# Kernel tuning notes

Hardware: AMD Instinct MI355X
Metric: run time of the kernel (lower is better)

The kernel has to match this reference:

```python
import jax, jax.numpy as jnp
import numpy as np

NB = 4
QN = -(2 ** (NB - 1))   # -8
QP = 2 ** (NB - 1) - 1  # 7
EPS = 1e-5


def _grad_scale(x, g):
    # forward: x, backward: grad * g (LSQ gradient scaling)
    return x * g + jax.lax.stop_gradient(x - x * g)


def _round_pass(x):
    # round with straight-through estimator
    return x + jax.lax.stop_gradient(jnp.round(x) - x)


def _lsq(v, alpha, qn, qp):
    # LSQ fake quantize-dequantize with learnable step size alpha
    g = 1.0 / np.sqrt(v.size * qp)
    a = _grad_scale(alpha, g)
    return _round_pass(jnp.clip(v / a, qn, qp)) * a


def _bn(x, g, b, m, v):
    # eval-mode BatchNorm2d over channel dim of NCHW
    s = (g * jax.lax.rsqrt(v + EPS))[None, :, None, None]
    return (x - m[None, :, None, None]) * s + b[None, :, None, None]


def _conv(x, w, stride, pad, groups):
    return jax.lax.conv_general_dilated(
        x, w, (stride, stride), pad,
        dimension_numbers=('NCHW', 'OIHW', 'NCHW'),
        feature_group_count=groups)


def setup_inputs() -> dict:
    key = jax.random.key(0)
    ks = jax.random.split(key, 4)
    inp, oup, hid = 96, 96, 576
    B, H, W = 32, 28, 28
    d = {}
    d['x'] = jax.random.normal(ks[0], (B, inp, H, W), jnp.float32)
    d['w1'] = jax.random.normal(ks[1], (hid, inp, 1, 1), jnp.float32) * 0.1
    d['w2'] = jax.random.normal(ks[2], (hid, 1, 3, 3), jnp.float32) * 0.1
    d['w3'] = jax.random.normal(ks[3], (oup, hid, 1, 1), jnp.float32) * 0.1
    for i, c in zip((1, 2, 3), (hid, hid, oup)):
        d[f'aw{i}'] = jnp.full((1,), 0.05, jnp.float32)  # weight step size
        d[f'ax{i}'] = jnp.full((1,), 0.5, jnp.float32)   # activation step size
        d[f'g{i}'] = jnp.ones((c,), jnp.float32)
        d[f'b{i}'] = jnp.zeros((c,), jnp.float32)
        d[f'm{i}'] = jnp.zeros((c,), jnp.float32)
        d[f'v{i}'] = jnp.ones((c,), jnp.float32)
    return d


def reference(x, w1, w2, w3, aw1, ax1, g1, b1, m1, v1,
              aw2, ax2, g2, b2, m2, v2, aw3, ax3, g3, b3, m3, v3):
    hid = w1.shape[0]
    # 1x1 expand conv (LSQ on activation and weight)
    h = _conv(_lsq(x, ax1, QN, QP), _lsq(w1, aw1, QN, QP), 1, [(0, 0), (0, 0)], 1)
    h = jnp.clip(_bn(h, g1, b1, m1, v1), 0.0, 6.0)
    # 3x3 depthwise conv, stride 1
    h = _conv(_lsq(h, ax2, QN, QP), _lsq(w2, aw2, QN, QP), 1, [(1, 1), (1, 1)], hid)
    h = jnp.clip(_bn(h, g2, b2, m2, v2), 0.0, 6.0)
    # 1x1 project conv
    h = _conv(_lsq(h, ax3, QN, QP), _lsq(w3, aw3, QN, QP), 1, [(0, 0), (0, 0)], 1)
    h = _bn(h, g3, b3, m3, v3)
    # identity residual (stride==1 and inp==oup)
    return x + h
```

## Files before the change

kernel.cpp:

```cpp
#include <hip/hip_runtime.h>

#define EPSF 1e-5f

typedef int    int4v   __attribute__((ext_vector_type(4)));
typedef float  float4v __attribute__((ext_vector_type(4)));

#define W1P_OFF  0
#define W3P_OFF  55296
#define W2D_OFF  110592
#define S1B1_OFF 202752
#define S2B2_OFF 207360
#define S3B3_OFF 211968

#define H1S 296
#define H2S 600

__device__ __forceinline__ float lsq_q(float v, float a) {
    float t = v / a;
    t = fminf(fmaxf(t, -8.0f), 7.0f);
    return rintf(t);
}

__device__ __forceinline__ long q8pack_w(const float* w, int base, const int* idx, float a) {
    unsigned long long v = 0;
    #pragma unroll
    for (int j = 0; j < 8; ++j) {
        int q = (int)lsq_q(w[base + idx[j]], a);
        v |= (unsigned long long)(q & 255) << (8 * j);
    }
    return (long)v;
}

__global__ __launch_bounds__(256)
void prep_w(const float* __restrict__ w1, const float* __restrict__ w2,
            const float* __restrict__ w3,
            const float* aw1, const float* ax1, const float* ax2,
            const float* aw2, const float* ax3, const float* aw3,
            const float* __restrict__ g1, const float* __restrict__ b1,
            const float* __restrict__ m1, const float* __restrict__ v1,
            const float* __restrict__ g2, const float* __restrict__ b2,
            const float* __restrict__ m2, const float* __restrict__ v2,
            const float* __restrict__ g3, const float* __restrict__ b3,
            const float* __restrict__ m3, const float* __restrict__ v3,
            long* __restrict__ w1p, long* __restrict__ w3p,
            long* __restrict__ w2d,
            float* __restrict__ s1b1, float* __restrict__ s2b2,
            float* __restrict__ s3b3) {
    int id = blockIdx.x * 256 + threadIdx.x;
    const int lin[8] = {0, 1, 2, 3, 4, 5, 6, 7};
    if (id < 6912) {
        int l = id & 63, t = id >> 6;
        int kc = t % 3, ct = t / 3;
        int co = ct * 16 + (l & 15);
        int ci0 = kc * 32 + (l >> 4) * 8;
        w1p[id] = q8pack_w(w1, co * 96 + ci0, lin, aw1[0]);
    } else if (id < 13824) {
        int i = id - 6912;
        int l = i & 63, t = i >> 6;
        int kc = t % 18, ct = t / 18;
        int co = ct * 16 + (l & 15);
        int ci0 = kc * 32 + (l >> 4) * 8;
        w3p[i] = q8pack_w(w3, co * 576 + ci0, lin, aw3[0]);
    } else if (id < 25344) {
        int i = id - 13824;
        int l = i & 63, t = i >> 6;
        int kc = t % 5, ct = t / 5;
        int quad = l >> 4, m = l & 15;
        int tap = kc * 2 + (quad >> 1);
        unsigned long long v = 0;
        if (tap <= 8) {
            int mh = m - (quad & 1) * 8;
            if (mh >= 0 && mh < 8) {
                int j = (mh >> 1) | ((mh & 1) << 2);
                int q = (int)lsq_q(w2[(ct * 16 + m) * 9 + tap], aw2[0]);
                v = (unsigned long long)(unsigned)(q & 255) << (8 * j);
            }
        }
        w2d[i] = (long)v;
    } else if (id < 25920) {
        int c = id - 25344;
        float s = g1[c] / sqrtf(v1[c] + EPSF);
        float A = aw1[0] * ax1[0];
        float inv = 1.0f / ax2[0];
        s1b1[c] = A * s * inv;
        s1b1[576 + c] = (b1[c] - m1[c] * s) * inv;
    } else if (id < 26496) {
        int c = id - 25920;
        float s = g2[c] / sqrtf(v2[c] + EPSF);
        float A = ax2[0] * aw2[0];
        float inv = 1.0f / ax3[0];
        s2b2[c] = A * s * inv;
        s2b2[576 + c] = (b2[c] - m2[c] * s) * inv;
    } else if (id < 26592) {
        int c = id - 26496;
        float s = g3[c] / sqrtf(v3[c] + EPSF);
        float A = ax3[0] * aw3[0];
        s3b3[c] = A * s;
        s3b3[96 + c] = b3[c] - m3[c] * s;
    }
}

__global__ __launch_bounds__(448, 4)
void fused_k(const float* __restrict__ x, const long* __restrict__ w1p,
             const long* __restrict__ w2d, const long* __restrict__ w3p,
             const float* __restrict__ ax1,
             const float* __restrict__ s1b1, const float* __restrict__ s2b2,
             const float* __restrict__ s3b3, float* __restrict__ out) {
    __shared__ __align__(16) signed char h1[120 * H1S];
    __shared__ __align__(16) signed char h2[64 * H2S];
    const int tid = threadIdx.x;
    const int w = tid >> 6, l = tid & 63;
    const int quad = l >> 4, c16 = l & 15;
    const int qh = quad >> 1, ql = quad & 1;
    const int b = blockIdx.x;
    const int r0 = blockIdx.y * 2;

    for (int i = tid; i < 120 * H1S / 16; i += 448)
        ((int4v*)h1)[i] = (int4v){0, 0, 0, 0};
    __syncthreads();

    {
        const int lp = w * 16 + c16;
        const int row = lp / 28, col = lp - (lp / 28) * 28;
        const int img_row = r0 - 1 + row;
        const bool valid = (unsigned)img_row < 28u;
        const int p = min(max(img_row, 0), 27) * 28 + col;
        const float inv1 = 1.0f / ax1[0];

        long bfr[3];
        #pragma unroll
        for (int kc = 0; kc < 3; ++kc) {
            const float* xs = x + (b * 96 + kc * 32 + quad * 8) * 784 + p;
            unsigned long long v = 0;
            #pragma unroll
            for (int j = 0; j < 8; ++j) {
                float t = xs[j * 784] * inv1;
                t = fminf(fmaxf(t, -8.0f), 7.0f);
                int q = (int)rintf(t);
                v |= (unsigned long long)(q & 255) << (8 * j);
            }
            bfr[kc] = (long)v;
        }
        const int pos_h = row * 30 + col + 1;
        #pragma unroll 4
        for (int ct = 0; ct < 36; ++ct) {
            int4v acc; acc[0] = 0; acc[1] = 0; acc[2] = 0; acc[3] = 0;
            #pragma unroll
            for (int kc = 0; kc < 3; ++kc)
                acc = __builtin_amdgcn_mfma_i32_16x16x32_i8(
                    w1p[(ct * 3 + kc) * 64 + l], bfr[kc], acc, 0, 0, 0);
            const int co0 = ct * 16 + quad * 4;
            float4v S = *(const float4v*)(s1b1 + co0);
            float4v B = *(const float4v*)(s1b1 + 576 + co0);
            int pk = 0;
            #pragma unroll
            for (int r = 0; r < 4; ++r) {
                float t = fmaf((float)acc[r], S[r], B[r]);
                t = fminf(fmaxf(t, 0.0f), 7.0f);
                pk |= ((int)rintf(t)) << (4 * r);
            }
            if (valid)
                *(unsigned short*)(h1 + pos_h * H1S + (co0 >> 1)) = (unsigned short)pk;
        }
    }
    __syncthreads();

    for (int t = w; t < 144; t += 7) {
        const int pt = t / 36, ct = t - (t / 36) * 36;
        const int pos = pt * 16 + c16;
        const int posc = min(pos, 55);
        const int row_in = posc / 28, col = posc - (posc / 28) * 28;
        const int choff = ct * 8 + ql * 4;
        int4v acc; acc[0] = 0; acc[1] = 0; acc[2] = 0; acc[3] = 0;
        #pragma unroll
        for (int kc = 0; kc < 5; ++kc) {
            int tap = kc * 2 + qh;
            tap = min(tap, 8);
            const int dh = tap / 3 - 1, dc = tap - (tap / 3) * 3 - 1;
            const int pos_h = (row_in + 1 + dh) * 30 + (col + 1 + dc);
            const unsigned v = *(const unsigned*)(h1 + pos_h * H1S + choff);
            const unsigned lo = v & 0x0F0F0F0Fu;
            const unsigned hi = (v >> 4) & 0x0F0F0F0Fu;
            const long bf = (long)(((unsigned long long)hi << 32) | lo);
            acc = __builtin_amdgcn_mfma_i32_16x16x32_i8(
                w2d[(ct * 5 + kc) * 64 + l], bf, acc, 0, 0, 0);
        }
        if (pos < 56) {
            const int c0 = ct * 16 + quad * 4;
            float4v S = *(const float4v*)(s2b2 + c0);
            float4v B = *(const float4v*)(s2b2 + 576 + c0);
            int pk = 0;
            #pragma unroll
            for (int r = 0; r < 4; ++r) {
                float tt = fmaf((float)acc[r], S[r], B[r]);
                tt = fminf(fmaxf(tt, 0.0f), 7.0f);
                pk |= ((int)rintf(tt)) << (8 * r);
            }
            *(int*)(h2 + pos * H2S + c0) = pk;
        }
    }
    __syncthreads();

    for (int t = w; t < 24; t += 7) {
        const int nt = t / 6, ct = t - (t / 6) * 6;
        int4v acc; acc[0] = 0; acc[1] = 0; acc[2] = 0; acc[3] = 0;
        const signed char* arow = h2 + (nt * 16 + c16) * H2S + quad * 8;
        #pragma unroll 6
        for (int kc = 0; kc < 18; ++kc)
            acc = __builtin_amdgcn_mfma_i32_16x16x32_i8(
                *(const long*)(arow + kc * 32),
                w3p[(ct * 18 + kc) * 64 + l], acc, 0, 0, 0);
        const int nloc = nt * 16 + quad * 4;
        if (nloc < 56) {
            const int co = ct * 16 + c16;
            const float S = s3b3[co], Bv = s3b3[96 + co];
            const int off = (b * 96 + co) * 784 + r0 * 28 + nloc;
            const float4v xr = *(const float4v*)(x + off);
            float4v o;
            #pragma unroll
            for (int r = 0; r < 4; ++r)
                o[r] = fmaf((float)acc[r], S, Bv) + xr[r];
            *(float4v*)(out + off) = o;
        }
    }
}

extern "C" void kernel_launch(void* const* d_in, const int* in_sizes, int n_in,
                              void* d_out, int out_size, void* d_ws, size_t ws_size,
                              hipStream_t stream) {
    const float* x   = (const float*)d_in[0];
    const float* w1  = (const float*)d_in[1];
    const float* w2  = (const float*)d_in[2];
    const float* w3  = (const float*)d_in[3];
    const float* aw1 = (const float*)d_in[4];
    const float* ax1 = (const float*)d_in[5];
    const float* g1  = (const float*)d_in[6];
    const float* b1  = (const float*)d_in[7];
    const float* m1  = (const float*)d_in[8];
    const float* v1  = (const float*)d_in[9];
    const float* aw2 = (const float*)d_in[10];
    const float* ax2 = (const float*)d_in[11];
    const float* g2  = (const float*)d_in[12];
    const float* b2  = (const float*)d_in[13];
    const float* m2  = (const float*)d_in[14];
    const float* v2  = (const float*)d_in[15];
    const float* aw3 = (const float*)d_in[16];
    const float* ax3 = (const float*)d_in[17];
    const float* g3  = (const float*)d_in[18];
    const float* b3  = (const float*)d_in[19];
    const float* m3  = (const float*)d_in[20];
    const float* v3  = (const float*)d_in[21];

    char* ws = (char*)d_ws;
    long* w1p = (long*)(ws + W1P_OFF);
    long* w3p = (long*)(ws + W3P_OFF);
    long* w2d = (long*)(ws + W2D_OFF);
    float* s1b1 = (float*)(ws + S1B1_OFF);
    float* s2b2 = (float*)(ws + S2B2_OFF);
    float* s3b3 = (float*)(ws + S3B3_OFF);

    float* out = (float*)d_out;

    prep_w<<<104, 256, 0, stream>>>(w1, w2, w3, aw1, ax1, ax2, aw2, ax3, aw3,
                                    g1, b1, m1, v1, g2, b2, m2, v2, g3, b3, m3, v3,
                                    w1p, w3p, w2d, s1b1, s2b2, s3b3);
    dim3 grid(32, 14);
    fused_k<<<grid, 448, 0, stream>>>(x, w1p, w2d, w3p, ax1, s1b1, s2b2, s3b3, out);
}
```

Measured before the change: 145.0 us.

## Split fused block into expand-conv kernel and depthwise+project kernel via global buffer

The expand 1x1 conv moves out of the fused kernel into its own kernel, which writes packed 4-bit activations to a global workspace in NHWC layout. The depthwise+project kernel then handles one output row per block and loads the needed halo rows from that buffer. This removes the redundant recomputation of halo rows in the expand conv (previously 4 rows computed per 2 output rows) and lets each kernel choose its own tiling and occupancy. The cost is an extra kernel launch and a global round trip for the intermediate, about 7 MB written and about 3x that read back, while the depthwise kernel now reads 3 halo rows for each output row.

Result: slower. 149.4 us (+3.1%).

```diff
diff --git a/kernel.cpp b/kernel.cpp
--- a/kernel.cpp
+++ b/kernel.cpp
@@ -5,14 +5,15 @@
 typedef int    int4v   __attribute__((ext_vector_type(4)));
 typedef float  float4v __attribute__((ext_vector_type(4)));
 
-#define W1P_OFF  0
-#define W3P_OFF  55296
-#define W2D_OFF  110592
-#define S1B1_OFF 202752
-#define S2B2_OFF 207360
-#define S3B3_OFF 211968
-
-#define H1S 296
+#define QH1N_OFF 0
+#define W1P_OFF  7225344
+#define W3P_OFF  7280640
+#define W2D_OFF  7335936
+#define S1B1_OFF 7428096
+#define S2B2_OFF 7432704
+#define S3B3_OFF 7437312
+
+#define H1S 304
 #define H2S 600
 
 __device__ __forceinline__ float lsq_q(float v, float a) {
@@ -21,11 +22,11 @@
     return rintf(t);
 }
 
-__device__ __forceinline__ long q8pack_w(const float* w, int base, const int* idx, float a) {
+__device__ __forceinline__ long q8pack_w(const float* w, int base, float a) {
     unsigned long long v = 0;
     #pragma unroll
     for (int j = 0; j < 8; ++j) {
-        int q = (int)lsq_q(w[base + idx[j]], a);
+        int q = (int)lsq_q(w[base + j], a);
         v |= (unsigned long long)(q & 255) << (8 * j);
     }
     return (long)v;
@@ -47,20 +48,19 @@
             float* __restrict__ s1b1, float* __restrict__ s2b2,
             float* __restrict__ s3b3) {
     int id = blockIdx.x * 256 + threadIdx.x;
-    const int lin[8] = {0, 1, 2, 3, 4, 5, 6, 7};
     if (id < 6912) {
         int l = id & 63, t = id >> 6;
         int kc = t % 3, ct = t / 3;
         int co = ct * 16 + (l & 15);
         int ci0 = kc * 32 + (l >> 4) * 8;
-        w1p[id] = q8pack_w(w1, co * 96 + ci0, lin, aw1[0]);
+        w1p[id] = q8pack_w(w1, co * 96 + ci0, aw1[0]);
     } else if (id < 13824) {
         int i = id - 6912;
         int l = i & 63, t = i >> 6;
         int kc = t % 18, ct = t / 18;
         int co = ct * 16 + (l & 15);
         int ci0 = kc * 32 + (l >> 4) * 8;
-        w3p[i] = q8pack_w(w3, co * 576 + ci0, lin, aw3[0]);
+        w3p[i] = q8pack_w(w3, co * 576 + ci0, aw3[0]);
     } else if (id < 25344) {
         int i = id - 13824;
         int l = i & 63, t = i >> 6;
@@ -100,109 +100,127 @@
     }
 }
 
-__global__ __launch_bounds__(448, 4)
-void fused_k(const float* __restrict__ x, const long* __restrict__ w1p,
-             const long* __restrict__ w2d, const long* __restrict__ w3p,
-             const float* __restrict__ ax1,
-             const float* __restrict__ s1b1, const float* __restrict__ s2b2,
-             const float* __restrict__ s3b3, float* __restrict__ out) {
-    __shared__ __align__(16) signed char h1[120 * H1S];
-    __shared__ __align__(16) signed char h2[64 * H2S];
+__global__ __launch_bounds__(256, 4)
+void conv1_k(const float* __restrict__ x, const long* __restrict__ w1p,
+             const float* __restrict__ ax1, const float* __restrict__ s1b1,
+             unsigned short* __restrict__ qh1n) {
+    const int tid = threadIdx.x;
+    const int w = tid >> 6, l = tid & 63;
+    const int quad = l >> 4, c16 = l & 15;
+    const int n0 = blockIdx.x * 64, cs = blockIdx.y;
+    const int n = n0 + w * 16 + c16;
+    const int bi = n / 784, p = n - bi * 784;
+    const float inv1 = 1.0f / ax1[0];
+
+    long bfr[3];
+    #pragma unroll
+    for (int kc = 0; kc < 3; ++kc) {
+        const float* xs = x + (bi * 96 + kc * 32 + quad * 8) * 784 + p;
+        unsigned long long v = 0;
+        #pragma unroll
+        for (int j = 0; j < 8; ++j) {
+            float t = xs[j * 784] * inv1;
+            t = fminf(fmaxf(t, -8.0f), 7.0f);
+            int q = (int)rintf(t);
+            v |= (unsigned long long)(q & 255) << (8 * j);
+        }
+        bfr[kc] = (long)v;
+    }
+
+    int4v acc[12];
+    #pragma unroll
+    for (int i = 0; i < 12; ++i) { acc[i][0] = 0; acc[i][1] = 0; acc[i][2] = 0; acc[i][3] = 0; }
+    #pragma unroll
+    for (int kc = 0; kc < 3; ++kc)
+        #pragma unroll
+        for (int ct = 0; ct < 12; ++ct)
+            acc[ct] = __builtin_amdgcn_mfma_i32_16x16x32_i8(
+                w1p[((cs * 12 + ct) * 3 + kc) * 64 + l], bfr[kc], acc[ct], 0, 0, 0);
+
+    #pragma unroll
+    for (int ct = 0; ct < 12; ++ct) {
+        const int co0 = cs * 192 + ct * 16 + quad * 4;
+        float4v S = *(const float4v*)(s1b1 + co0);
+        float4v B = *(const float4v*)(s1b1 + 576 + co0);
+        int pk = 0;
+        #pragma unroll
+        for (int r = 0; r < 4; ++r) {
+            float t = fmaf((float)acc[ct][r], S[r], B[r]);
+            t = fminf(fmaxf(t, 0.0f), 7.0f);
+            pk |= ((int)rintf(t)) << (4 * r);
+        }
+        qh1n[n * 144 + cs * 48 + ct * 4 + quad] = (unsigned short)pk;
+    }
+}
+
+__global__ __launch_bounds__(512, 4)
+void dwc3_k(const unsigned char* __restrict__ qh1n, const long* __restrict__ w2d,
+            const long* __restrict__ w3p, const float* __restrict__ x,
+            const float* __restrict__ s2b2, const float* __restrict__ s3b3,
+            float* __restrict__ out) {
+    __shared__ __align__(16) unsigned char h1[90 * H1S];
+    __shared__ __align__(16) signed char  h2[32 * H2S];
     const int tid = threadIdx.x;
     const int w = tid >> 6, l = tid & 63;
     const int quad = l >> 4, c16 = l & 15;
     const int qh = quad >> 1, ql = quad & 1;
     const int b = blockIdx.x;
-    const int r0 = blockIdx.y * 2;
-
-    for (int i = tid; i < 120 * H1S / 16; i += 448)
-        ((int4v*)h1)[i] = (int4v){0, 0, 0, 0};
+    const int r = blockIdx.y;
+
+    #pragma unroll
+    for (int i = 0; i < 4; ++i) {
+        const int idx = tid + 512 * i;
+        if (idx < 1620) {
+            const int rs = idx / 18, ch = idx - rs * 18;
+            const int tr = rs / 30, colh = rs - tr * 30;
+            const int col = colh - 1, ir = r - 1 + tr;
+            int4v v = {0, 0, 0, 0};
+            if ((unsigned)ir < 28u && (unsigned)col < 28u)
+                v = *(const int4v*)(qh1n + (b * 784 + ir * 28 + col) * 288 + ch * 16);
+            *(int4v*)(h1 + rs * H1S + ch * 16) = v;
+        }
+    }
     __syncthreads();
 
-    {
-        const int lp = w * 16 + c16;
-        const int row = lp / 28, col = lp - (lp / 28) * 28;
-        const int img_row = r0 - 1 + row;
-        const bool valid = (unsigned)img_row < 28u;
-        const int p = min(max(img_row, 0), 27) * 28 + col;
-        const float inv1 = 1.0f / ax1[0];
-
-        long bfr[3];
-        #pragma unroll
-        for (int kc = 0; kc < 3; ++kc) {
-            const float* xs = x + (b * 96 + kc * 32 + quad * 8) * 784 + p;
-            unsigned long long v = 0;
-            #pragma unroll
-            for (int j = 0; j < 8; ++j) {
-                float t = xs[j * 784] * inv1;
-                t = fminf(fmaxf(t, -8.0f), 7.0f);
-                int q = (int)rintf(t);
-                v |= (unsigned long long)(q & 255) << (8 * j);
-            }
-            bfr[kc] = (long)v;
-        }
-        const int pos_h = row * 30 + col + 1;
-        #pragma unroll 4
-        for (int ct = 0; ct < 36; ++ct) {
-            int4v acc; acc[0] = 0; acc[1] = 0; acc[2] = 0; acc[3] = 0;
-            #pragma unroll
-            for (int kc = 0; kc < 3; ++kc)
-                acc = __builtin_amdgcn_mfma_i32_16x16x32_i8(
-                    w1p[(ct * 3 + kc) * 64 + l], bfr[kc], acc, 0, 0, 0);
-            const int co0 = ct * 16 + quad * 4;
-            float4v S = *(const float4v*)(s1b1 + co0);
-            float4v B = *(const float4v*)(s1b1 + 576 + co0);
-            int pk = 0;
-            #pragma unroll
-            for (int r = 0; r < 4; ++r) {
-                float t = fmaf((float)acc[r], S[r], B[r]);
-                t = fminf(fmaxf(t, 0.0f), 7.0f);
-                pk |= ((int)rintf(t)) << (4 * r);
-            }
-            if (valid)
-                *(unsigned short*)(h1 + pos_h * H1S + (co0 >> 1)) = (unsigned short)pk;
-        }
-    }
-    __syncthreads();
-
-    for (int t = w; t < 144; t += 7) {
-        const int pt = t / 36, ct = t - (t / 36) * 36;
+    int boff[5];
+    #pragma unroll
+    for (int kc = 0; kc < 5; ++kc) {
+        int tap = kc * 2 + qh;
+        tap = min(tap, 8);
+        const int dh = tap / 3 - 1, dc = tap - (tap / 3) * 3 - 1;
+        boff[kc] = (dh * 30 + dc) * H1S;
+    }
+    for (int t = w; t < 72; t += 8) {
+        const int pt = (t >= 36) ? 1 : 0, ct = t - pt * 36;
         const int pos = pt * 16 + c16;
-        const int posc = min(pos, 55);
-        const int row_in = posc / 28, col = posc - (posc / 28) * 28;
-        const int choff = ct * 8 + ql * 4;
+        const int col = min(pos, 27);
+        const unsigned char* sbase = h1 + (31 + col) * H1S + ct * 8 + ql * 4;
         int4v acc; acc[0] = 0; acc[1] = 0; acc[2] = 0; acc[3] = 0;
         #pragma unroll
         for (int kc = 0; kc < 5; ++kc) {
-            int tap = kc * 2 + qh;
-            tap = min(tap, 8);
-            const int dh = tap / 3 - 1, dc = tap - (tap / 3) * 3 - 1;
-            const int pos_h = (row_in + 1 + dh) * 30 + (col + 1 + dc);
-            const unsigned v = *(const unsigned*)(h1 + pos_h * H1S + choff);
+            const unsigned v = *(const unsigned*)(sbase + boff[kc]);
             const unsigned lo = v & 0x0F0F0F0Fu;
             const unsigned hi = (v >> 4) & 0x0F0F0F0Fu;
             const long bf = (long)(((unsigned long long)hi << 32) | lo);
             acc = __builtin_amdgcn_mfma_i32_16x16x32_i8(
                 w2d[(ct * 5 + kc) * 64 + l], bf, acc, 0, 0, 0);
         }
-        if (pos < 56) {
-            const int c0 = ct * 16 + quad * 4;
-            float4v S = *(const float4v*)(s2b2 + c0);
-            float4v B = *(const float4v*)(s2b2 + 576 + c0);
-            int pk = 0;
-            #pragma unroll
-            for (int r = 0; r < 4; ++r) {
-                float tt = fmaf((float)acc[r], S[r], B[r]);
-                tt = fminf(fmaxf(tt, 0.0f), 7.0f);
-                pk |= ((int)rintf(tt)) << (8 * r);
-            }
-            *(int*)(h2 + pos * H2S + c0) = pk;
-        }
+        const int c0 = ct * 16 + quad * 4;
+        float4v S = *(const float4v*)(s2b2 + c0);
+        float4v B = *(const float4v*)(s2b2 + 576 + c0);
+        int pk = 0;
+        #pragma unroll
+        for (int rr = 0; rr < 4; ++rr) {
+            float tt = fmaf((float)acc[rr], S[rr], B[rr]);
+            tt = fminf(fmaxf(tt, 0.0f), 7.0f);
+            pk |= ((int)rintf(tt)) << (8 * rr);
+        }
+        *(int*)(h2 + pos * H2S + c0) = pk;
     }
     __syncthreads();
 
-    for (int t = w; t < 24; t += 7) {
-        const int nt = t / 6, ct = t - (t / 6) * 6;
+    for (int t = w; t < 12; t += 8) {
+        const int nt = t / 6, ct = t - nt * 6;
         int4v acc; acc[0] = 0; acc[1] = 0; acc[2] = 0; acc[3] = 0;
         const signed char* arow = h2 + (nt * 16 + c16) * H2S + quad * 8;
         #pragma unroll 6
@@ -211,15 +229,15 @@
                 *(const long*)(arow + kc * 32),
                 w3p[(ct * 18 + kc) * 64 + l], acc, 0, 0, 0);
         const int nloc = nt * 16 + quad * 4;
-        if (nloc < 56) {
+        if (nloc < 28) {
             const int co = ct * 16 + c16;
             const float S = s3b3[co], Bv = s3b3[96 + co];
-            const int off = (b * 96 + co) * 784 + r0 * 28 + nloc;
+            const int off = (b * 96 + co) * 784 + r * 28 + nloc;
             const float4v xr = *(const float4v*)(x + off);
             float4v o;
             #pragma unroll
-            for (int r = 0; r < 4; ++r)
-                o[r] = fmaf((float)acc[r], S, Bv) + xr[r];
+            for (int rr = 0; rr < 4; ++rr)
+                o[rr] = fmaf((float)acc[rr], S, Bv) + xr[rr];
             *(float4v*)(out + off) = o;
         }
     }
@@ -252,6 +270,7 @@
     const float* v3  = (const float*)d_in[21];
 
     char* ws = (char*)d_ws;
+    unsigned char* qh1n = (unsigned char*)(ws + QH1N_OFF);
     long* w1p = (long*)(ws + W1P_OFF);
     long* w3p = (long*)(ws + W3P_OFF);
     long* w2d = (long*)(ws + W2D_OFF);
@@ -264,6 +283,8 @@
     prep_w<<<104, 256, 0, stream>>>(w1, w2, w3, aw1, ax1, ax2, aw2, ax3, aw3,
                                     g1, b1, m1, v1, g2, b2, m2, v2, g3, b3, m3, v3,
                                     w1p, w3p, w2d, s1b1, s2b2, s3b3);
-    dim3 grid(32, 14);
-    fused_k<<<grid, 448, 0, stream>>>(x, w1p, w2d, w3p, ax1, s1b1, s2b2, s3b3, out);
-}
+    dim3 g1d(392, 3);
+    conv1_k<<<g1d, 256, 0, stream>>>(x, w1p, ax1, s1b1, (unsigned short*)qh1n);
+    dim3 g2d(32, 28);
+    dwc3_k<<<g2d, 512, 0, stream>>>(qh1n, w2d, w3p, x, s2b2, s3b3, out);
+}
```

## Interleave two tiles per wave with split accumulators and drop full h1 zeroing

Applied to the files above, without the earlier changes.

The depthwise and projection stages now give each wave two independent tiles at once, with two accumulator chains per tile. This breaks the serial MFMA dependency and exposes more instruction-level parallelism. The full shared-memory zero-fill of h1 and its barrier are replaced by writing zeros for invalid rows inline and zeroing only the left and right padding columns. The h1 row stride changes from 296 to 292, likely to reduce LDS bank conflicts, and the 16-byte alignment on h1 is dropped. In exchange, register pressure rises under the 448x4 launch bounds, and any h1 pad entries not covered by the new zeroing could be read as garbage.

Measured after the change: 151.0 us. 4.2% more time.

```diff
diff --git a/kernel.cpp b/kernel.cpp
--- a/kernel.cpp
+++ b/kernel.cpp
@@ -12,7 +12,7 @@
 #define S2B2_OFF 207360
 #define S3B3_OFF 211968
 
-#define H1S 296
+#define H1S 292
 #define H2S 600
 
 __device__ __forceinline__ float lsq_q(float v, float a) {
@@ -21,11 +21,11 @@
     return rintf(t);
 }
 
-__device__ __forceinline__ long q8pack_w(const float* w, int base, const int* idx, float a) {
+__device__ __forceinline__ long q8pack_w(const float* w, int base, float a) {
     unsigned long long v = 0;
     #pragma unroll
     for (int j = 0; j < 8; ++j) {
-        int q = (int)lsq_q(w[base + idx[j]], a);
+        int q = (int)lsq_q(w[base + j], a);
         v |= (unsigned long long)(q & 255) << (8 * j);
     }
     return (long)v;
@@ -47,20 +47,19 @@
             float* __restrict__ s1b1, float* __restrict__ s2b2,
             float* __restrict__ s3b3) {
     int id = blockIdx.x * 256 + threadIdx.x;
-    const int lin[8] = {0, 1, 2, 3, 4, 5, 6, 7};
     if (id < 6912) {
         int l = id & 63, t = id >> 6;
         int kc = t % 3, ct = t / 3;
         int co = ct * 16 + (l & 15);
         int ci0 = kc * 32 + (l >> 4) * 8;
-        w1p[id] = q8pack_w(w1, co * 96 + ci0, lin, aw1[0]);
+        w1p[id] = q8pack_w(w1, co * 96 + ci0, aw1[0]);
     } else if (id < 13824) {
         int i = id - 6912;
         int l = i & 63, t = i >> 6;
         int kc = t % 18, ct = t / 18;
         int co = ct * 16 + (l & 15);
         int ci0 = kc * 32 + (l >> 4) * 8;
-        w3p[i] = q8pack_w(w3, co * 576 + ci0, lin, aw3[0]);
+        w3p[i] = q8pack_w(w3, co * 576 + ci0, aw3[0]);
     } else if (id < 25344) {
         int i = id - 13824;
         int l = i & 63, t = i >> 6;
@@ -106,7 +105,7 @@
              const float* __restrict__ ax1,
              const float* __restrict__ s1b1, const float* __restrict__ s2b2,
              const float* __restrict__ s3b3, float* __restrict__ out) {
-    __shared__ __align__(16) signed char h1[120 * H1S];
+    __shared__ signed char h1[120 * H1S];
     __shared__ __align__(16) signed char h2[64 * H2S];
     const int tid = threadIdx.x;
     const int w = tid >> 6, l = tid & 63;
@@ -115,10 +114,6 @@
     const int b = blockIdx.x;
     const int r0 = blockIdx.y * 2;
 
-    for (int i = tid; i < 120 * H1S / 16; i += 448)
-        ((int4v*)h1)[i] = (int4v){0, 0, 0, 0};
-    __syncthreads();
-
     {
         const int lp = w * 16 + c16;
         const int row = lp / 28, col = lp - (lp / 28) * 28;
@@ -159,68 +154,141 @@
                 t = fminf(fmaxf(t, 0.0f), 7.0f);
                 pk |= ((int)rintf(t)) << (4 * r);
             }
-            if (valid)
-                *(unsigned short*)(h1 + pos_h * H1S + (co0 >> 1)) = (unsigned short)pk;
-        }
+            pk = valid ? pk : 0;
+            *(unsigned short*)(h1 + pos_h * H1S + (co0 >> 1)) = (unsigned short)pk;
+        }
+    }
+    for (int i = tid; i < 576; i += 448) {
+        const int q = i / 72, word = i - q * 72;
+        const int pos_h = (q >> 1) * 30 + (q & 1) * 29;
+        *(int*)(h1 + pos_h * H1S + word * 4) = 0;
     }
     __syncthreads();
 
-    for (int t = w; t < 144; t += 7) {
-        const int pt = t / 36, ct = t - (t / 36) * 36;
-        const int pos = pt * 16 + c16;
-        const int posc = min(pos, 55);
-        const int row_in = posc / 28, col = posc - (posc / 28) * 28;
-        const int choff = ct * 8 + ql * 4;
-        int4v acc; acc[0] = 0; acc[1] = 0; acc[2] = 0; acc[3] = 0;
+    int boff[5];
+    #pragma unroll
+    for (int kc = 0; kc < 5; ++kc) {
+        int tap = kc * 2 + qh;
+        tap = min(tap, 8);
+        const int dh = tap / 3 - 1, dc = tap - (tap / 3) * 3 - 1;
+        boff[kc] = (dh * 30 + dc) * H1S;
+    }
+    for (int t = w; t < 144; t += 14) {
+        const int t2r = t + 7;
+        const int t2 = (t2r < 144) ? t2r : t;
+        const int ptA = t / 36,  ctA = t - ptA * 36;
+        const int ptB = t2 / 36, ctB = t2 - ptB * 36;
+        const int posA = ptA * 16 + c16, posB = ptB * 16 + c16;
+        const int colA = min(posA, 55) % 28 + (min(posA, 55) / 28) * 0;
+        const int pA = min(posA, 55), pB = min(posB, 55);
+        const int rA = pA / 28, cA = pA - rA * 28;
+        const int rB = pB / 28, cB = pB - rB * 28;
+        (void)colA;
+        const signed char* baseA = h1 + ((rA + 1) * 30 + cA + 1) * H1S + ctA * 8 + ql * 4;
+        const signed char* baseB = h1 + ((rB + 1) * 30 + cB + 1) * H1S + ctB * 8 + ql * 4;
+        int4v a0; a0[0] = 0; a0[1] = 0; a0[2] = 0; a0[3] = 0;
+        int4v a1 = a0, b0 = a0, b1 = a0;
         #pragma unroll
         for (int kc = 0; kc < 5; ++kc) {
-            int tap = kc * 2 + qh;
-            tap = min(tap, 8);
-            const int dh = tap / 3 - 1, dc = tap - (tap / 3) * 3 - 1;
-            const int pos_h = (row_in + 1 + dh) * 30 + (col + 1 + dc);
-            const unsigned v = *(const unsigned*)(h1 + pos_h * H1S + choff);
-            const unsigned lo = v & 0x0F0F0F0Fu;
-            const unsigned hi = (v >> 4) & 0x0F0F0F0Fu;
-            const long bf = (long)(((unsigned long long)hi << 32) | lo);
-            acc = __builtin_amdgcn_mfma_i32_16x16x32_i8(
-                w2d[(ct * 5 + kc) * 64 + l], bf, acc, 0, 0, 0);
-        }
-        if (pos < 56) {
-            const int c0 = ct * 16 + quad * 4;
+            const unsigned vA = *(const unsigned*)(baseA + boff[kc]);
+            const unsigned vB = *(const unsigned*)(baseB + boff[kc]);
+            const long bfA = (long)((((unsigned long long)((vA >> 4) & 0x0F0F0F0Fu)) << 32)
+                                    | (vA & 0x0F0F0F0Fu));
+            const long bfB = (long)((((unsigned long long)((vB >> 4) & 0x0F0F0F0Fu)) << 32)
+                                    | (vB & 0x0F0F0F0Fu));
+            const long wA = w2d[(ctA * 5 + kc) * 64 + l];
+            const long wB = w2d[(ctB * 5 + kc) * 64 + l];
+            if (kc < 3) {
+                a0 = __builtin_amdgcn_mfma_i32_16x16x32_i8(wA, bfA, a0, 0, 0, 0);
+                b0 = __builtin_amdgcn_mfma_i32_16x16x32_i8(wB, bfB, b0, 0, 0, 0);
+            } else {
+                a1 = __builtin_amdgcn_mfma_i32_16x16x32_i8(wA, bfA, a1, 0, 0, 0);
+                b1 = __builtin_amdgcn_mfma_i32_16x16x32_i8(wB, bfB, b1, 0, 0, 0);
+            }
+        }
+        #pragma unroll
+        for (int rr = 0; rr < 4; ++rr) { a0[rr] += a1[rr]; b0[rr] += b1[rr]; }
+        {
+            const int c0 = ctA * 16 + quad * 4;
             float4v S = *(const float4v*)(s2b2 + c0);
             float4v B = *(const float4v*)(s2b2 + 576 + c0);
             int pk = 0;
             #pragma unroll
-            for (int r = 0; r < 4; ++r) {
-                float tt = fmaf((float)acc[r], S[r], B[r]);
+            for (int rr = 0; rr < 4; ++rr) {
+                float tt = fmaf((float)a0[rr], S[rr], B[rr]);
                 tt = fminf(fmaxf(tt, 0.0f), 7.0f);
-                pk |= ((int)rintf(tt)) << (8 * r);
-            }
-            *(int*)(h2 + pos * H2S + c0) = pk;
+                pk |= ((int)rintf(tt)) << (8 * rr);
+            }
+            if (posA < 56) *(int*)(h2 + posA * H2S + c0) = pk;
+        }
+        {
+            const int c0 = ctB * 16 + quad * 4;
+            float4v S = *(const float4v*)(s2b2 + c0);
+            float4v B = *(const float4v*)(s2b2 + 576 + c0);
+            int pk = 0;
+            #pragma unroll
+            for (int rr = 0; rr < 4; ++rr) {
+                float tt = fmaf((float)b0[rr], S[rr], B[rr]);
+                tt = fminf(fmaxf(tt, 0.0f), 7.0f);
+                pk |= ((int)rintf(tt)) << (8 * rr);
+            }
+            if (posB < 56 && t2r < 144) *(int*)(h2 + posB * H2S + c0) = pk;
         }
     }
     __syncthreads();
 
-    for (int t = w; t < 24; t += 7) {
-        const int nt = t / 6, ct = t - (t / 6) * 6;
-        int4v acc; acc[0] = 0; acc[1] = 0; acc[2] = 0; acc[3] = 0;
-        const signed char* arow = h2 + (nt * 16 + c16) * H2S + quad * 8;
+    for (int t = w; t < 24; t += 14) {
+        const int t2r = t + 7;
+        const int t2 = (t2r < 24) ? t2r : t;
+        const int ntA = t / 6,  ctA = t - ntA * 6;
+        const int ntB = t2 / 6, ctB = t2 - ntB * 6;
+        const signed char* arowA = h2 + (ntA * 16 + c16) * H2S + quad * 8;
+        const signed char* arowB = h2 + (ntB * 16 + c16) * H2S + quad * 8;
+        int4v a0; a0[0] = 0; a0[1] = 0; a0[2] = 0; a0[3] = 0;
+        int4v a1 = a0, b0 = a0, b1 = a0;
         #pragma unroll 6
-        for (int kc = 0; kc < 18; ++kc)
-            acc = __builtin_amdgcn_mfma_i32_16x16x32_i8(
-                *(const long*)(arow + kc * 32),
-                w3p[(ct * 18 + kc) * 64 + l], acc, 0, 0, 0);
-        const int nloc = nt * 16 + quad * 4;
-        if (nloc < 56) {
-            const int co = ct * 16 + c16;
-            const float S = s3b3[co], Bv = s3b3[96 + co];
-            const int off = (b * 96 + co) * 784 + r0 * 28 + nloc;
-            const float4v xr = *(const float4v*)(x + off);
-            float4v o;
-            #pragma unroll
-            for (int r = 0; r < 4; ++r)
-                o[r] = fmaf((float)acc[r], S, Bv) + xr[r];
-            *(float4v*)(out + off) = o;
+        for (int kc = 0; kc < 18; ++kc) {
+            const long xA = *(const long*)(arowA + kc * 32);
+            const long xB = *(const long*)(arowB + kc * 32);
+            const long wA = w3p[(ctA * 18 + kc) * 64 + l];
+            const long wB = w3p[(ctB * 18 + kc) * 64 + l];
+            if (kc < 9) {
+                a0 = __builtin_amdgcn_mfma_i32_16x16x32_i8(xA, wA, a0, 0, 0, 0);
+                b0 = __builtin_amdgcn_mfma_i32_16x16x32_i8(xB, wB, b0, 0, 0, 0);
+            } else {
+                a1 = __builtin_amdgcn_mfma_i32_16x16x32_i8(xA, wA, a1, 0, 0, 0);
+                b1 = __builtin_amdgcn_mfma_i32_16x16x32_i8(xB, wB, b1, 0, 0, 0);
+            }
+        }
+        #pragma unroll
+        for (int rr = 0; rr < 4; ++rr) { a0[rr] += a1[rr]; b0[rr] += b1[rr]; }
+        {
+            const int nloc = ntA * 16 + quad * 4;
+            if (nloc < 56) {
+                const int co = ctA * 16 + c16;
+                const float S = s3b3[co], Bv = s3b3[96 + co];
+                const int off = (b * 96 + co) * 784 + r0 * 28 + nloc;
+                const float4v xr = *(const float4v*)(x + off);
+                float4v o;
+                #pragma unroll
+                for (int rr = 0; rr < 4; ++rr)
+                    o[rr] = fmaf((float)a0[rr], S, Bv) + xr[rr];
+                *(float4v*)(out + off) = o;
+            }
+        }
+        if (t2r < 24) {
+            const int nloc = ntB * 16 + quad * 4;
+            if (nloc < 56) {
+                const int co = ctB * 16 + c16;
+                const float S = s3b3[co], Bv = s3b3[96 + co];
+                const int off = (b * 96 + co) * 784 + r0 * 28 + nloc;
+                const float4v xr = *(const float4v*)(x + off);
+                float4v o;
+                #pragma unroll
+                for (int rr = 0; rr < 4; ++rr)
+                    o[rr] = fmaf((float)b0[rr], S, Bv) + xr[rr];
+                *(float4v*)(out + off) = o;
+            }
         }
     }
 }
```

## Shrink fused tile to one output row and pack h2 as 4-bit

Applied to the files above, without the earlier changes.

Each block now computes one output row instead of two, so the grid doubles to 32x28 and the h1 halo tile shrinks to three input rows. The intermediate h2 is stored as packed 4-bit nibbles like h1, with w3 bytes permuted to match the nibble unpacking, which halves h2 shared memory. Only the halo columns are zeroed instead of the whole buffer, and occupancy is raised to 7 blocks per CU. The cost is more recomputation of the halo rows for the 1x1 expand conv (3 rows per output row instead of 4 per 2), plus extra unpack work in the project stage.

New measurement: 162.3 us. 12.0% more time.

```diff
diff --git a/kernel.cpp b/kernel.cpp
--- a/kernel.cpp
+++ b/kernel.cpp
@@ -13,7 +13,7 @@
 #define S3B3_OFF 211968
 
 #define H1S 296
-#define H2S 600
+#define H2S 296
 
 __device__ __forceinline__ float lsq_q(float v, float a) {
     float t = v / a;
@@ -21,7 +21,17 @@
     return rintf(t);
 }
 
-__device__ __forceinline__ long q8pack_w(const float* w, int base, const int* idx, float a) {
+__device__ __forceinline__ long q8pack_w(const float* w, int base, float a) {
+    unsigned long long v = 0;
+    #pragma unroll
+    for (int j = 0; j < 8; ++j) {
+        int q = (int)lsq_q(w[base + j], a);
+        v |= (unsigned long long)(q & 255) << (8 * j);
+    }
+    return (long)v;
+}
+
+__device__ __forceinline__ long q8pack_wp(const float* w, int base, const int* idx, float a) {
     unsigned long long v = 0;
     #pragma unroll
     for (int j = 0; j < 8; ++j) {
@@ -47,20 +57,20 @@
             float* __restrict__ s1b1, float* __restrict__ s2b2,
             float* __restrict__ s3b3) {
     int id = blockIdx.x * 256 + threadIdx.x;
-    const int lin[8] = {0, 1, 2, 3, 4, 5, 6, 7};
     if (id < 6912) {
         int l = id & 63, t = id >> 6;
         int kc = t % 3, ct = t / 3;
         int co = ct * 16 + (l & 15);
         int ci0 = kc * 32 + (l >> 4) * 8;
-        w1p[id] = q8pack_w(w1, co * 96 + ci0, lin, aw1[0]);
+        w1p[id] = q8pack_w(w1, co * 96 + ci0, aw1[0]);
     } else if (id < 13824) {
         int i = id - 6912;
         int l = i & 63, t = i >> 6;
         int kc = t % 18, ct = t / 18;
         int co = ct * 16 + (l & 15);
         int ci0 = kc * 32 + (l >> 4) * 8;
-        w3p[i] = q8pack_w(w3, co * 576 + ci0, lin, aw3[0]);
+        const int perm[8] = {0, 2, 4, 6, 1, 3, 5, 7};
+        w3p[i] = q8pack_wp(w3, co * 576 + ci0, perm, aw3[0]);
     } else if (id < 25344) {
         int i = id - 13824;
         int l = i & 63, t = i >> 6;
@@ -100,31 +110,28 @@
     }
 }
 
-__global__ __launch_bounds__(448, 4)
+__global__ __launch_bounds__(448, 7)
 void fused_k(const float* __restrict__ x, const long* __restrict__ w1p,
              const long* __restrict__ w2d, const long* __restrict__ w3p,
              const float* __restrict__ ax1,
              const float* __restrict__ s1b1, const float* __restrict__ s2b2,
              const float* __restrict__ s3b3, float* __restrict__ out) {
-    __shared__ __align__(16) signed char h1[120 * H1S];
-    __shared__ __align__(16) signed char h2[64 * H2S];
+    __shared__ unsigned char h1[90 * H1S];
+    __shared__ unsigned char h2[32 * H2S];
     const int tid = threadIdx.x;
     const int w = tid >> 6, l = tid & 63;
     const int quad = l >> 4, c16 = l & 15;
     const int qh = quad >> 1, ql = quad & 1;
     const int b = blockIdx.x;
-    const int r0 = blockIdx.y * 2;
-
-    for (int i = tid; i < 120 * H1S / 16; i += 448)
-        ((int4v*)h1)[i] = (int4v){0, 0, 0, 0};
-    __syncthreads();
-
-    {
-        const int lp = w * 16 + c16;
-        const int row = lp / 28, col = lp - (lp / 28) * 28;
-        const int img_row = r0 - 1 + row;
-        const bool valid = (unsigned)img_row < 28u;
-        const int p = min(max(img_row, 0), 27) * 28 + col;
+    const int r = blockIdx.y;
+
+    if (w < 6) {
+        const int sp = w * 16 + c16;
+        const int tr = sp / 28, col = sp - tr * 28;
+        const int ir = r - 1 + tr;
+        const bool vrow = (unsigned)ir < 28u;
+        const bool vpos = sp < 84;
+        const int p = min(max(ir, 0), 27) * 28 + col;
         const float inv1 = 1.0f / ax1[0];
 
         long bfr[3];
@@ -141,7 +148,7 @@
             }
             bfr[kc] = (long)v;
         }
-        const int pos_h = row * 30 + col + 1;
+        const int pos_h = tr * 30 + col + 1;
         #pragma unroll 4
         for (int ct = 0; ct < 36; ++ct) {
             int4v acc; acc[0] = 0; acc[1] = 0; acc[2] = 0; acc[3] = 0;
@@ -154,72 +161,82 @@
             float4v B = *(const float4v*)(s1b1 + 576 + co0);
             int pk = 0;
             #pragma unroll
-            for (int r = 0; r < 4; ++r) {
-                float t = fmaf((float)acc[r], S[r], B[r]);
+            for (int rr = 0; rr < 4; ++rr) {
+                float t = fmaf((float)acc[rr], S[rr], B[rr]);
                 t = fminf(fmaxf(t, 0.0f), 7.0f);
-                pk |= ((int)rintf(t)) << (4 * r);
+                pk |= ((int)rintf(t)) << (4 * rr);
             }
-            if (valid)
-                *(unsigned short*)(h1 + pos_h * H1S + (co0 >> 1)) = (unsigned short)pk;
-        }
+            pk = vrow ? pk : 0;
+            if (vpos)
+                *(unsigned short*)(h1 + pos_h * H1S + ct * 8 + quad * 2) = (unsigned short)pk;
+        }
+    }
+    if (tid < 432) {
+        const int tr = tid / 144, rem = tid - tr * 144;
+        const int colh = (rem / 72) * 29, word = rem - (rem / 72) * 72;
+        *(int*)(h1 + (tr * 30 + colh) * H1S + word * 4) = 0;
     }
     __syncthreads();
 
-    for (int t = w; t < 144; t += 7) {
-        const int pt = t / 36, ct = t - (t / 36) * 36;
+    int boff[5];
+    #pragma unroll
+    for (int kc = 0; kc < 5; ++kc) {
+        int tap = kc * 2 + qh;
+        tap = min(tap, 8);
+        const int dh = tap / 3 - 1, dc = tap - (tap / 3) * 3 - 1;
+        boff[kc] = (dh * 30 + dc) * H1S;
+    }
+    for (int t = w; t < 72; t += 7) {
+        const int pt = (t >= 36) ? 1 : 0, ct = t - pt * 36;
         const int pos = pt * 16 + c16;
-        const int posc = min(pos, 55);
-        const int row_in = posc / 28, col = posc - (posc / 28) * 28;
-        const int choff = ct * 8 + ql * 4;
+        const int col = min(pos, 27);
+        const unsigned char* sbase = h1 + (30 + col + 1) * H1S + ct * 8 + ql * 4;
         int4v acc; acc[0] = 0; acc[1] = 0; acc[2] = 0; acc[3] = 0;
         #pragma unroll
         for (int kc = 0; kc < 5; ++kc) {
-            int tap = kc * 2 + qh;
-            tap = min(tap, 8);
-            const int dh = tap / 3 - 1, dc = tap - (tap / 3) * 3 - 1;
-            const int pos_h = (row_in + 1 + dh) * 30 + (col + 1 + dc);
-            const unsigned v = *(const unsigned*)(h1 + pos_h * H1S + choff);
-            const unsigned lo = v & 0x0F0F0F0Fu;
-            const unsigned hi = (v >> 4) & 0x0F0F0F0Fu;
-            const long bf = (long)(((unsigned long long)hi << 32) | lo);
+            const unsigned v = *(const unsigned*)(sbase + boff[kc]);
+            const long bf = (long)((((unsigned long long)((v >> 4) & 0x0F0F0F0Fu)) << 32)
+                                   | (v & 0x0F0F0F0Fu));
             acc = __builtin_amdgcn_mfma_i32_16x16x32_i8(
                 w2d[(ct * 5 + kc) * 64 + l], bf, acc, 0, 0, 0);
         }
-        if (pos < 56) {
-            const int c0 = ct * 16 + quad * 4;
-            float4v S = *(const float4v*)(s2b2 + c0);
-            float4v B = *(const float4v*)(s2b2 + 576 + c0);
-            int pk = 0;
-            #pragma unroll
-            for (int r = 0; r < 4; ++r) {
-                float tt = fmaf((float)acc[r], S[r], B[r]);
-                tt = fminf(fmaxf(tt, 0.0f), 7.0f);
-                pk |= ((int)rintf(tt)) << (8 * r);
-            }
-            *(int*)(h2 + pos * H2S + c0) = pk;
-        }
+        const int c0 = ct * 16 + quad * 4;
+        float4v S = *(const float4v*)(s2b2 + c0);
+        float4v B = *(const float4v*)(s2b2 + 576 + c0);
+        int pk = 0;
+        #pragma unroll
+        for (int rr = 0; rr < 4; ++rr) {
+            float tt = fmaf((float)acc[rr], S[rr], B[rr]);
+            tt = fminf(fmaxf(tt, 0.0f), 7.0f);
+            pk |= ((int)rintf(tt)) << (4 * rr);
+        }
+        if (pos < 28)
+            *(unsigned short*)(h2 + pos * H2S + ct * 8 + quad * 2) = (unsigned short)pk;
     }
     __syncthreads();
 
-    for (int t = w; t < 24; t += 7) {
-        const int nt = t / 6, ct = t - (t / 6) * 6;
+    for (int t = w; t < 12; t += 7) {
+        const int nt = t / 6, ct = t - nt * 6;
+        const unsigned char* arow = h2 + (nt * 16 + c16) * H2S + quad * 4;
         int4v acc; acc[0] = 0; acc[1] = 0; acc[2] = 0; acc[3] = 0;
-        const signed char* arow = h2 + (nt * 16 + c16) * H2S + quad * 8;
         #pragma unroll 6
-        for (int kc = 0; kc < 18; ++kc)
+        for (int kc = 0; kc < 18; ++kc) {
+            const unsigned v = *(const unsigned*)(arow + kc * 16);
+            const long a = (long)((((unsigned long long)((v >> 4) & 0x0F0F0F0Fu)) << 32)
+                                  | (v & 0x0F0F0F0Fu));
             acc = __builtin_amdgcn_mfma_i32_16x16x32_i8(
-                *(const long*)(arow + kc * 32),
-                w3p[(ct * 18 + kc) * 64 + l], acc, 0, 0, 0);
+                a, w3p[(ct * 18 + kc) * 64 + l], acc, 0, 0, 0);
+        }
         const int nloc = nt * 16 + quad * 4;
-        if (nloc < 56) {
+        if (nloc < 28) {
             const int co = ct * 16 + c16;
             const float S = s3b3[co], Bv = s3b3[96 + co];
-            const int off = (b * 96 + co) * 784 + r0 * 28 + nloc;
+            const int off = (b * 96 + co) * 784 + r * 28 + nloc;
             const float4v xr = *(const float4v*)(x + off);
             float4v o;
             #pragma unroll
-            for (int r = 0; r < 4; ++r)
-                o[r] = fmaf((float)acc[r], S, Bv) + xr[r];
+            for (int rr = 0; rr < 4; ++rr)
+                o[rr] = fmaf((float)acc[rr], S, Bv) + xr[rr];
             *(float4v*)(out + off) = o;
         }
     }
@@ -264,6 +281,6 @@
     prep_w<<<104, 256, 0, stream>>>(w1, w2, w3, aw1, ax1, ax2, aw2, ax3, aw3,
                                     g1, b1, m1, v1, g2, b2, m2, v2, g3, b3, m3, v3,
                                     w1p, w3p, w2d, s1b1, s2b2, s3b3);
-    dim3 grid(32, 14);
+    dim3 grid(32, 28);
     fused_k<<<grid, 448, 0, stream>>>(x, w1p, w2d, w3p, ax1, s1b1, s2b2, s3b3, out);
 }
```
